# Kernel tuning notes

Hardware: AMD Instinct MI355X
Metric: run time of the kernel (lower is better)

The kernel has to match this reference:

```python
import jax, jax.numpy as jnp
import numpy as np
import math

EMBED_DIM = 256
N_HEAD = 8
N_LEVELS = 4
N_POINTS = 4
HEAD_DIM = EMBED_DIM // N_HEAD
TOTAL_POINTS = N_HEAD * N_LEVELS * N_POINTS
SPATIAL = np.array([[100, 100], [50, 50], [25, 25], [13, 13]], dtype=np.int32)
BS = 2
LEN_Q = int(SPATIAL.prod(1).sum())  # 13294, encoder self-attention
LEN_V = LEN_Q


def setup_inputs() -> dict:
    key = jax.random.key(0)
    ks = jax.random.split(key, 12)
    s = 1.0 / math.sqrt(EMBED_DIM)
    inp = {
        'query': jax.random.normal(ks[0], (BS, LEN_Q, EMBED_DIM), jnp.float32),
        'reference_points': jax.random.uniform(ks[1], (BS, LEN_Q, N_LEVELS, 2), jnp.float32),
        'value': jax.random.normal(ks[2], (BS, LEN_V, EMBED_DIM), jnp.float32),
        'value_spatial_shapes': jnp.asarray(SPATIAL),
        'W_value': jax.random.normal(ks[3], (EMBED_DIM, EMBED_DIM), jnp.float32) * s,
        'b_value': jnp.zeros((EMBED_DIM,), jnp.float32),
        'W_off': jax.random.normal(ks[4], (TOTAL_POINTS * 2, EMBED_DIM), jnp.float32) * 0.01,
        'b_off': jax.random.normal(ks[5], (TOTAL_POINTS * 2,), jnp.float32),
        'W_attn': jax.random.normal(ks[6], (TOTAL_POINTS, EMBED_DIM), jnp.float32) * s,
        'b_attn': jnp.zeros((TOTAL_POINTS,), jnp.float32),
        'W_out': jax.random.normal(ks[7], (EMBED_DIM, EMBED_DIM), jnp.float32) * s,
        'b_out': jnp.zeros((EMBED_DIM,), jnp.float32),
        'zeta': jnp.ones((1, 1, 1, HEAD_DIM), jnp.float32),  # search_type='embed'
    }
    return inp


def _grid_sample_bilinear(img, gx, gy):
    """img: [B,H,W,c]; gx,gy: [B,Q,P] normalized to [-1,1].
    align_corners=False, padding_mode='zeros' (matches F.grid_sample)."""
    B, H, W, c = img.shape
    x = (gx + 1.0) * (0.5 * W) - 0.5
    y = (gy + 1.0) * (0.5 * H) - 0.5
    x0 = jnp.floor(x)
    y0 = jnp.floor(y)
    wx = (x - x0)[..., None]
    wy = (y - y0)[..., None]
    flat = img.reshape(B, H * W, c)

    def gather(xi, yi):
        m = (xi >= 0) & (xi < W) & (yi >= 0) & (yi < H)
        xi_c = jnp.clip(xi, 0, W - 1).astype(jnp.int32)
        yi_c = jnp.clip(yi, 0, H - 1).astype(jnp.int32)
        idx = (yi_c * W + xi_c).reshape(B, -1, 1)
        v = jnp.take_along_axis(flat, idx, axis=1).reshape(B, *xi.shape[1:], c)
        return v * m[..., None]

    v00 = gather(x0, y0)
    v01 = gather(x0 + 1, y0)
    v10 = gather(x0, y0 + 1)
    v11 = gather(x0 + 1, y0 + 1)
    return (v00 * (1 - wx) * (1 - wy) + v01 * wx * (1 - wy)
            + v10 * (1 - wx) * wy + v11 * wx * wy)


def reference(query, reference_points, value, value_spatial_shapes,
              W_value, b_value, W_off, b_off, W_attn, b_attn, W_out, b_out, zeta):
    bs, Len_q, _ = query.shape
    Len_v = value.shape[1]
    shapes = np.asarray(value_spatial_shapes)  # static ints

    # value projection + sparse gate (zeta, not pruned/searched)
    v = value @ W_value.T + b_value
    v = v.reshape(bs, Len_v, N_HEAD, HEAD_DIM) * zeta  # [bs,Lv,h,c]

    # sampling offsets and attention weights from query
    off = (query @ W_off.T + b_off).reshape(bs, Len_q, N_HEAD, N_LEVELS, N_POINTS, 2)
    attn = (query @ W_attn.T + b_attn).reshape(bs, Len_q, N_HEAD, N_LEVELS * N_POINTS)
    attn = jax.nn.softmax(attn, axis=-1).reshape(bs, Len_q, N_HEAD, N_LEVELS, N_POINTS)

    # reference_points last dim == 2 branch
    normalizer = jnp.asarray(shapes[:, ::-1], jnp.float32).reshape(1, 1, 1, N_LEVELS, 1, 2)  # (W,H)
    loc = reference_points.reshape(bs, Len_q, 1, N_LEVELS, 1, 2) + off / normalizer
    grids = 2.0 * loc - 1.0  # [bs,Lq,h,L,P,2]

    B = bs * N_HEAD
    out = jnp.zeros((B, Len_q, HEAD_DIM), jnp.float32)
    start = 0
    for lvl in range(N_LEVELS):
        h, w = int(shapes[lvl, 0]), int(shapes[lvl, 1])
        # [bs, h*w, nh, c] -> [bs*nh, h, w, c]
        v_l = v[:, start:start + h * w].transpose(0, 2, 1, 3).reshape(B, h, w, HEAD_DIM)
        g = grids[:, :, :, lvl].transpose(0, 2, 1, 3, 4).reshape(B, Len_q, N_POINTS, 2)
        samp = _grid_sample_bilinear(v_l, g[..., 0], g[..., 1])  # [B,Lq,P,c]
        a_l = attn[:, :, :, lvl].transpose(0, 2, 1, 3).reshape(B, Len_q, N_POINTS)
        out = out + jnp.einsum('bqpc,bqp->bqc', samp, a_l)
        start += h * w

    out = out.reshape(bs, N_HEAD, Len_q, HEAD_DIM).transpose(0, 2, 1, 3).reshape(bs, Len_q, EMBED_DIM)
    return out @ W_out.T + b_out
```

## Files before the change

### kernel.cpp

```cpp
#include <hip/hip_runtime.h>


#define LQ    13294
#define NTOK  26588
#define NE    6806528

typedef unsigned short ushort_t;
typedef __attribute__((ext_vector_type(8))) short short8;
typedef __attribute__((ext_vector_type(8))) unsigned short ushort8_t;
typedef __attribute__((ext_vector_type(4))) float float4_t;

__device__ __forceinline__ ushort_t f2b(float f) {
    unsigned int x = __float_as_uint(f);
    return (ushort_t)((x + 0x7fffu + ((x >> 16) & 1u)) >> 16);
}

__device__ __forceinline__ void gload16(const void* g, void* l) {
    __builtin_amdgcn_global_load_lds(
        (const __attribute__((address_space(1))) unsigned int*)g,
        (__attribute__((address_space(3))) unsigned int*)l, 16, 0, 0);
}

__device__ __forceinline__ void cvt_seg(const float* __restrict__ s,
                                        ushort_t* __restrict__ d,
                                        int n4, int gid, int stride) {
    const float4_t* s4 = (const float4_t*)s;
    for (int i = gid; i < n4; i += stride) {
        float4_t f = s4[i];
        ushort4 o;
        o.x = f2b(f.x); o.y = f2b(f.y); o.z = f2b(f.z); o.w = f2b(f.w);
        *(ushort4*)(d + (long)i * 4) = o;
    }
}

__global__ __launch_bounds__(256) void cvt_k(
    const float* q, const float* v, const float* Wv, const float* Wo,
    const float* Wa, const float* Wout,
    ushort_t* q_bf, ushort_t* v_bf, ushort_t* Wv_bf, ushort_t* WoWa_bf,
    ushort_t* Wout_bf)
{
    const int gid = blockIdx.x * 256 + threadIdx.x;
    const int stride = gridDim.x * 256;
    cvt_seg(q,    q_bf,            NE / 4,     gid, stride);
    cvt_seg(v,    v_bf,            NE / 4,     gid, stride);
    cvt_seg(Wv,   Wv_bf,           65536 / 4,  gid, stride);
    cvt_seg(Wo,   WoWa_bf,         65536 / 4,  gid, stride);
    cvt_seg(Wa,   WoWa_bf + 65536, 32768 / 4,  gid, stride);
    cvt_seg(Wout, Wout_bf,         65536 / 4,  gid, stride);
}

__device__ __forceinline__ void gemm_tile(
    const ushort_t* __restrict__ A,
    const ushort_t* __restrict__ W,
    int m0, int n0,
    ushort_t* Asb, ushort_t* Bs, float4_t acc[2][4])
{
    const int tid = threadIdx.x;
    const int w  = tid >> 6;
    const int ln = tid & 63;
    const int lr = ln >> 2;
    const int lc = (ln & 3) * 8;

    const ushort_t* gB = W + (long)(n0 + w * 16 + lr) * 256 + lc;
    #pragma unroll
    for (int kt = 0; kt < 8; kt++)
        gload16(gB + kt * 32, Bs + kt * 2048 + w * 512);

    const ushort_t* gA0 = A + (long)(m0 + w * 32 + lr) * 256 + lc;
    const ushort_t* gA1 = gA0 + 16 * 256;
    gload16(gA0, Asb + (w * 2 + 0) * 512);
    gload16(gA1, Asb + (w * 2 + 1) * 512);
    __syncthreads();

    const int krow = (ln >> 4) * 8;
    const int fr   = ln & 15;

    #pragma unroll
    for (int kt = 0; kt < 8; kt++) {
        const int cur = (kt & 1) * 4096;
        if (kt < 7) {
            const int nxt = 4096 - cur;
            gload16(gA0 + (kt + 1) * 32, Asb + nxt + (w * 2 + 0) * 512);
            gload16(gA1 + (kt + 1) * 32, Asb + nxt + (w * 2 + 1) * 512);
        }
        short8 af[2], bfr[4];
        #pragma unroll
        for (int i = 0; i < 2; i++)
            af[i] = *(const short8*)(Asb + cur + (w * 32 + i * 16 + fr) * 32 + krow);
        #pragma unroll
        for (int j = 0; j < 4; j++)
            bfr[j] = *(const short8*)(Bs + kt * 2048 + (j * 16 + fr) * 32 + krow);
        #pragma unroll
        for (int i = 0; i < 2; i++)
            #pragma unroll
            for (int j = 0; j < 4; j++)
                acc[i][j] = __builtin_amdgcn_mfma_f32_16x16x32_bf16(af[i], bfr[j], acc[i][j], 0, 0, 0);
        __syncthreads();
    }
}

__global__ __launch_bounds__(256) void gemm_fused_k(
    const ushort_t* __restrict__ q_bf, const ushort_t* __restrict__ v_bf,
    const ushort_t* __restrict__ Wv,   const ushort_t* __restrict__ WoWa,
    const float* __restrict__ b_value, const float* __restrict__ b_off,
    const float* __restrict__ b_attn,  const float* __restrict__ zeta,
    ushort_t* __restrict__ vproj, float* __restrict__ oa)
{
    __shared__ __align__(16) ushort_t Asb[8192];
    __shared__ __align__(16) ushort_t Bs[16384];

    const int z = blockIdx.z;
    const int bid = blockIdx.x;
    int x, y;
    if (z == 0) {
        if (bid >= 832) return;
        int id = (bid & 7) * 104 + (bid >> 3);
        x = id >> 2; y = id & 3;
    } else {
        int id = (bid & 7) * 156 + (bid >> 3);
        x = id / 6; y = id - x * 6;
    }
    const int m0 = x * 128;
    const int n0 = y * 64;

    float4_t acc[2][4] = {};
    gemm_tile(z ? q_bf : v_bf, z ? WoWa : Wv, m0, n0, Asb, Bs, acc);

    const int tid = threadIdx.x;
    const int w = tid >> 6, ln = tid & 63;
    const int col = ln & 15;
    const int rq  = (ln >> 4) * 4;
    #pragma unroll
    for (int j = 0; j < 4; j++) {
        int n = n0 + j * 16 + col;
        if (z == 0) {
            float bz = b_value[n];
            float zz = zeta[n & 31];
            long hbase = (long)(n >> 5) * NTOK;
            #pragma unroll
            for (int i = 0; i < 2; i++) {
                #pragma unroll
                for (int r = 0; r < 4; r++) {
                    int m = m0 + w * 32 + i * 16 + rq + r;
                    if (m < NTOK)
                        vproj[(hbase + m) * 32 + (n & 31)] = f2b((acc[i][j][r] + bz) * zz);
                }
            }
        } else {
            float bz = (n < 256) ? b_off[n] : b_attn[n - 256];
            #pragma unroll
            for (int i = 0; i < 2; i++) {
                #pragma unroll
                for (int r = 0; r < 4; r++) {
                    int m = m0 + w * 32 + i * 16 + rq + r;
                    if (m < NTOK) oa[(long)m * 384 + n] = acc[i][j][r] + bz;
                }
            }
        }
    }
}

__global__ __launch_bounds__(256) void gemm_out_k(
    const ushort_t* __restrict__ A,
    const ushort_t* __restrict__ W,
    const float* __restrict__ bias,
    float* __restrict__ C)
{
    __shared__ __align__(16) ushort_t Asb[8192];
    __shared__ __align__(16) ushort_t Bs[16384];

    const int bid = blockIdx.x;
    int id = (bid & 7) * 104 + (bid >> 3);
    const int m0 = (id >> 2) * 128;
    const int n0 = (id & 3) * 64;

    float4_t acc[2][4] = {};
    gemm_tile(A, W, m0, n0, Asb, Bs, acc);

    const int tid = threadIdx.x;
    const int w = tid >> 6, ln = tid & 63;
    const int col = ln & 15;
    const int rq  = (ln >> 4) * 4;
    #pragma unroll
    for (int j = 0; j < 4; j++) {
        int n = n0 + j * 16 + col;
        float bz = bias[n];
        #pragma unroll
        for (int i = 0; i < 2; i++) {
            #pragma unroll
            for (int r = 0; r < 4; r++) {
                int m = m0 + w * 32 + i * 16 + rq + r;
                if (m < NTOK) C[(long)m * 256 + n] = acc[i][j][r] + bz;
            }
        }
    }
}

__global__ __launch_bounds__(512) void sample_k(
    const float* __restrict__ refp,
    const ushort_t* __restrict__ v,
    const float* __restrict__ oa,
    ushort_t* __restrict__ outp)
{
    __shared__ __align__(16) int   p_ofs[1152][4];
    __shared__ __align__(16) float p_w[1152][4];
    const int tid = threadIdx.x;
    const int tok = tid >> 6;
    const int ln  = tid & 63;
    const long t  = (long)blockIdx.x * 8 + tok;
    const bool valid = (t < NTOK);
    const int b = (t >= LQ) ? 1 : 0;

    if (valid) {
        #pragma unroll
        for (int half = 0; half < 2; half++) {
            const int h  = (ln >> 4) + half * 4;
            const int pi = ln & 15;
            const int lvl = pi >> 2;
            const int Wi  = (lvl == 0) ? 100 : (lvl == 1) ? 50 : (lvl == 2) ? 25 : 13;
            const int st  = (lvl == 0) ? 0 : (lvl == 1) ? 10000 : (lvl == 2) ? 12500 : 13125;
            const float Wf = (float)Wi;

            float lg = oa[t * 384 + 256 + h * 16 + pi];
            float smax = lg;
            #pragma unroll
            for (int d = 1; d < 16; d <<= 1) smax = fmaxf(smax, __shfl_xor(smax, d, 64));
            float ex = __expf(lg - smax);
            float sm = ex;
            #pragma unroll
            for (int d = 1; d < 16; d <<= 1) sm += __shfl_xor(sm, d, 64);
            const float a = ex / sm;

            float ox = oa[t * 384 + h * 32 + pi * 2];
            float oy = oa[t * 384 + h * 32 + pi * 2 + 1];
            float rx = refp[t * 8 + lvl * 2];
            float ry = refp[t * 8 + lvl * 2 + 1];

            float x = rx * Wf + ox - 0.5f;
            float y = ry * Wf + oy - 0.5f;
            float xf = floorf(x), yf = floorf(y);
            float wx = x - xf, wy = y - yf;
            int x0 = (int)xf, y0 = (int)yf;

            float mx0 = ((unsigned)x0       < (unsigned)Wi) ? (1.f - wx) : 0.f;
            float mx1 = ((unsigned)(x0 + 1) < (unsigned)Wi) ? wx         : 0.f;
            float my0 = ((unsigned)y0       < (unsigned)Wi) ? (1.f - wy) * a : 0.f;
            float my1 = ((unsigned)(y0 + 1) < (unsigned)Wi) ? wy * a         : 0.f;
            int x0c = min(max(x0, 0), Wi - 1);
            int x1c = min(max(x0 + 1, 0), Wi - 1);
            int y0c = min(max(y0, 0), Wi - 1);
            int y1c = min(max(y0 + 1, 0), Wi - 1);

            const int hb = h * NTOK + b * LQ + st;
            int r0 = hb + y0c * Wi, r1 = hb + y1c * Wi;
            const int u  = tok * 128 + half * 64 + ln;
            const int su = u + (u >> 3);
            p_ofs[su][0] = (r0 + x0c) << 6;
            p_ofs[su][1] = (r0 + x1c) << 6;
            p_ofs[su][2] = (r1 + x0c) << 6;
            p_ofs[su][3] = (r1 + x1c) << 6;
            p_w[su][0] = mx0 * my0;
            p_w[su][1] = mx1 * my0;
            p_w[su][2] = mx0 * my1;
            p_w[su][3] = mx1 * my1;
        }
    }
    __syncthreads();

    if (!valid) return;

    const int h = ln >> 3, s = (ln >> 2) & 1, g = ln & 3;
    const char* vb = (const char*)v;
    const unsigned go = g * 16;
    const int base = tok * 128 + h * 16 + s * 8;
    const int skb  = base + (base >> 3);
    float4_t accA = {0.f, 0.f, 0.f, 0.f};
    float4_t accB = {0.f, 0.f, 0.f, 0.f};

    #pragma unroll 2
    for (int p = 0; p < 8; p++) {
        int4     o  = *(const int4*)p_ofs[skb + p];
        float4_t w4 = *(const float4_t*)p_w[skb + p];
        uint4 u00 = *(const uint4*)(vb + (unsigned)(o.x + go));
        uint4 u01 = *(const uint4*)(vb + (unsigned)(o.y + go));
        uint4 u10 = *(const uint4*)(vb + (unsigned)(o.z + go));
        uint4 u11 = *(const uint4*)(vb + (unsigned)(o.w + go));
        #define ACC8(U, WGT) \
            accA[0] += (WGT) * __uint_as_float((U).x << 16); \
            accA[1] += (WGT) * __uint_as_float((U).x & 0xffff0000u); \
            accA[2] += (WGT) * __uint_as_float((U).y << 16); \
            accA[3] += (WGT) * __uint_as_float((U).y & 0xffff0000u); \
            accB[0] += (WGT) * __uint_as_float((U).z << 16); \
            accB[1] += (WGT) * __uint_as_float((U).z & 0xffff0000u); \
            accB[2] += (WGT) * __uint_as_float((U).w << 16); \
            accB[3] += (WGT) * __uint_as_float((U).w & 0xffff0000u);
        ACC8(u00, w4.x)
        ACC8(u01, w4.y)
        ACC8(u10, w4.z)
        ACC8(u11, w4.w)
        #undef ACC8
    }

    #pragma unroll
    for (int c = 0; c < 4; c++) {
        accA[c] += __shfl_down(accA[c], 4, 64);
        accB[c] += __shfl_down(accB[c], 4, 64);
    }

    if ((ln & 4) == 0) {
        ushort8_t o8;
        o8[0] = f2b(accA[0]); o8[1] = f2b(accA[1]);
        o8[2] = f2b(accA[2]); o8[3] = f2b(accA[3]);
        o8[4] = f2b(accB[0]); o8[5] = f2b(accB[1]);
        o8[6] = f2b(accB[2]); o8[7] = f2b(accB[3]);
        *(ushort8_t*)(outp + t * 256 + h * 32 + g * 8) = o8;
    }
}

extern "C" void kernel_launch(void* const* d_in, const int* in_sizes, int n_in,
                              void* d_out, int out_size, void* d_ws, size_t ws_size,
                              hipStream_t stream)
{
    char* ws = (char*)d_ws;
    ushort_t* vproj   = (ushort_t*)ws;
    float*    oa      = (float*)(ws + (long)NE * 2);
    ushort_t* q_bf    = (ushort_t*)(ws + (long)NE * 2 + (long)NTOK * 1536);
    ushort_t* outpre  = q_bf;
    ushort_t* v_bf    = q_bf + NE;
    ushort_t* Wv_bf   = v_bf + NE;
    ushort_t* WoWa_bf = Wv_bf + 65536;
    ushort_t* Wout_bf = WoWa_bf + 98304;

    cvt_k<<<1024, 256, 0, stream>>>(
        (const float*)d_in[0], (const float*)d_in[2], (const float*)d_in[4],
        (const float*)d_in[6], (const float*)d_in[8], (const float*)d_in[10],
        q_bf, v_bf, Wv_bf, WoWa_bf, Wout_bf);

    gemm_fused_k<<<dim3(1248, 1, 2), 256, 0, stream>>>(
        q_bf, v_bf, Wv_bf, WoWa_bf,
        (const float*)d_in[5], (const float*)d_in[7], (const float*)d_in[9],
        (const float*)d_in[12], vproj, oa);

    sample_k<<<3324, 512, 0, stream>>>(
        (const float*)d_in[1], vproj, oa, outpre);

    gemm_out_k<<<832, 256, 0, stream>>>(
        outpre, Wout_bf, (const float*)d_in[11], (float*)d_out);
}
```

Measured before the change: 224.5 us.

## Split sampling kernel per head and simplify GEMM tile staging

The sampling kernel now gives each block one head for eight tokens, so each wave covers one (token, head) pair. Every lane computes its own point's softmax weight, bilinear offsets and four gathers directly, replacing the shared-memory staging of offsets and weights. The per-point partial sums are then reduced across lanes with a shuffle tree, and the grid grows eightfold. Separately, the GEMM tile drops the full B preload and the A double buffering in favour of a plain per-k-step load-sync-compute loop with much smaller LDS buffers, which may raise occupancy but exposes load latency.

```diff
diff --git a/kernel.cpp b/kernel.cpp
--- a/kernel.cpp
+++ b/kernel.cpp
@@ -53,7 +53,7 @@
     const ushort_t* __restrict__ A,
     const ushort_t* __restrict__ W,
     int m0, int n0,
-    ushort_t* Asb, ushort_t* Bs, float4_t acc[2][4])
+    ushort_t* As, ushort_t* Bs, float4_t acc[2][4])
 {
     const int tid = threadIdx.x;
     const int w  = tid >> 6;
@@ -61,35 +61,29 @@
     const int lr = ln >> 2;
     const int lc = (ln & 3) * 8;
 
-    const ushort_t* gB = W + (long)(n0 + w * 16 + lr) * 256 + lc;
-    #pragma unroll
-    for (int kt = 0; kt < 8; kt++)
-        gload16(gB + kt * 32, Bs + kt * 2048 + w * 512);
-
+    ushort_t* lA0 = As + (w * 2 + 0) * 512;
+    ushort_t* lA1 = As + (w * 2 + 1) * 512;
+    ushort_t* lB  = Bs + w * 512;
     const ushort_t* gA0 = A + (long)(m0 + w * 32 + lr) * 256 + lc;
     const ushort_t* gA1 = gA0 + 16 * 256;
-    gload16(gA0, Asb + (w * 2 + 0) * 512);
-    gload16(gA1, Asb + (w * 2 + 1) * 512);
-    __syncthreads();
+    const ushort_t* gB  = W + (long)(n0 + w * 16 + lr) * 256 + lc;
 
     const int krow = (ln >> 4) * 8;
     const int fr   = ln & 15;
 
-    #pragma unroll
-    for (int kt = 0; kt < 8; kt++) {
-        const int cur = (kt & 1) * 4096;
-        if (kt < 7) {
-            const int nxt = 4096 - cur;
-            gload16(gA0 + (kt + 1) * 32, Asb + nxt + (w * 2 + 0) * 512);
-            gload16(gA1 + (kt + 1) * 32, Asb + nxt + (w * 2 + 1) * 512);
-        }
+    for (int k0 = 0; k0 < 256; k0 += 32) {
+        gload16(gA0 + k0, lA0);
+        gload16(gA1 + k0, lA1);
+        gload16(gB  + k0, lB);
+        __syncthreads();
+
         short8 af[2], bfr[4];
         #pragma unroll
         for (int i = 0; i < 2; i++)
-            af[i] = *(const short8*)(Asb + cur + (w * 32 + i * 16 + fr) * 32 + krow);
+            af[i] = *(const short8*)(As + (w * 32 + i * 16 + fr) * 32 + krow);
         #pragma unroll
         for (int j = 0; j < 4; j++)
-            bfr[j] = *(const short8*)(Bs + kt * 2048 + (j * 16 + fr) * 32 + krow);
+            bfr[j] = *(const short8*)(Bs + (j * 16 + fr) * 32 + krow);
         #pragma unroll
         for (int i = 0; i < 2; i++)
             #pragma unroll
@@ -106,8 +100,8 @@
     const float* __restrict__ b_attn,  const float* __restrict__ zeta,
     ushort_t* __restrict__ vproj, float* __restrict__ oa)
 {
-    __shared__ __align__(16) ushort_t Asb[8192];
-    __shared__ __align__(16) ushort_t Bs[16384];
+    __shared__ __align__(16) ushort_t As[128 * 32];
+    __shared__ __align__(16) ushort_t Bs[64 * 32];
 
     const int z = blockIdx.z;
     const int bid = blockIdx.x;
@@ -124,7 +118,7 @@
     const int n0 = y * 64;
 
     float4_t acc[2][4] = {};
-    gemm_tile(z ? q_bf : v_bf, z ? WoWa : Wv, m0, n0, Asb, Bs, acc);
+    gemm_tile(z ? q_bf : v_bf, z ? WoWa : Wv, m0, n0, As, Bs, acc);
 
     const int tid = threadIdx.x;
     const int w = tid >> 6, ln = tid & 63;
@@ -166,8 +160,8 @@
     const float* __restrict__ bias,
     float* __restrict__ C)
 {
-    __shared__ __align__(16) ushort_t Asb[8192];
-    __shared__ __align__(16) ushort_t Bs[16384];
+    __shared__ __align__(16) ushort_t As[128 * 32];
+    __shared__ __align__(16) ushort_t Bs[64 * 32];
 
     const int bid = blockIdx.x;
     int id = (bid & 7) * 104 + (bid >> 3);
@@ -175,7 +169,7 @@
     const int n0 = (id & 3) * 64;
 
     float4_t acc[2][4] = {};
-    gemm_tile(A, W, m0, n0, Asb, Bs, acc);
+    gemm_tile(A, W, m0, n0, As, Bs, acc);
 
     const int tid = threadIdx.x;
     const int w = tid >> 6, ln = tid & 63;
@@ -202,112 +196,88 @@
     const float* __restrict__ oa,
     ushort_t* __restrict__ outp)
 {
-    __shared__ __align__(16) int   p_ofs[1152][4];
-    __shared__ __align__(16) float p_w[1152][4];
+    const int bid = blockIdx.x;
+    const int h   = bid & 7;
     const int tid = threadIdx.x;
-    const int tok = tid >> 6;
-    const int ln  = tid & 63;
-    const long t  = (long)blockIdx.x * 8 + tok;
-    const bool valid = (t < NTOK);
-    const int b = (t >= LQ) ? 1 : 0;
-
-    if (valid) {
-        #pragma unroll
-        for (int half = 0; half < 2; half++) {
-            const int h  = (ln >> 4) + half * 4;
-            const int pi = ln & 15;
-            const int lvl = pi >> 2;
-            const int Wi  = (lvl == 0) ? 100 : (lvl == 1) ? 50 : (lvl == 2) ? 25 : 13;
-            const int st  = (lvl == 0) ? 0 : (lvl == 1) ? 10000 : (lvl == 2) ? 12500 : 13125;
-            const float Wf = (float)Wi;
-
-            float lg = oa[t * 384 + 256 + h * 16 + pi];
-            float smax = lg;
-            #pragma unroll
-            for (int d = 1; d < 16; d <<= 1) smax = fmaxf(smax, __shfl_xor(smax, d, 64));
-            float ex = __expf(lg - smax);
-            float sm = ex;
-            #pragma unroll
-            for (int d = 1; d < 16; d <<= 1) sm += __shfl_xor(sm, d, 64);
-            const float a = ex / sm;
-
-            float ox = oa[t * 384 + h * 32 + pi * 2];
-            float oy = oa[t * 384 + h * 32 + pi * 2 + 1];
-            float rx = refp[t * 8 + lvl * 2];
-            float ry = refp[t * 8 + lvl * 2 + 1];
-
-            float x = rx * Wf + ox - 0.5f;
-            float y = ry * Wf + oy - 0.5f;
-            float xf = floorf(x), yf = floorf(y);
-            float wx = x - xf, wy = y - yf;
-            int x0 = (int)xf, y0 = (int)yf;
-
-            float mx0 = ((unsigned)x0       < (unsigned)Wi) ? (1.f - wx) : 0.f;
-            float mx1 = ((unsigned)(x0 + 1) < (unsigned)Wi) ? wx         : 0.f;
-            float my0 = ((unsigned)y0       < (unsigned)Wi) ? (1.f - wy) * a : 0.f;
-            float my1 = ((unsigned)(y0 + 1) < (unsigned)Wi) ? wy * a         : 0.f;
-            int x0c = min(max(x0, 0), Wi - 1);
-            int x1c = min(max(x0 + 1, 0), Wi - 1);
-            int y0c = min(max(y0, 0), Wi - 1);
-            int y1c = min(max(y0 + 1, 0), Wi - 1);
-
-            const int hb = h * NTOK + b * LQ + st;
-            int r0 = hb + y0c * Wi, r1 = hb + y1c * Wi;
-            const int u  = tok * 128 + half * 64 + ln;
-            const int su = u + (u >> 3);
-            p_ofs[su][0] = (r0 + x0c) << 6;
-            p_ofs[su][1] = (r0 + x1c) << 6;
-            p_ofs[su][2] = (r1 + x0c) << 6;
-            p_ofs[su][3] = (r1 + x1c) << 6;
-            p_w[su][0] = mx0 * my0;
-            p_w[su][1] = mx1 * my0;
-            p_w[su][2] = mx0 * my1;
-            p_w[su][3] = mx1 * my1;
-        }
-    }
-    __syncthreads();
-
-    if (!valid) return;
-
-    const int h = ln >> 3, s = (ln >> 2) & 1, g = ln & 3;
+    const long t  = (long)(bid >> 3) * 8 + (tid >> 6);
+    if (t >= NTOK) return;
+    const int b  = (t >= LQ) ? 1 : 0;
+    const int ln = tid & 63;
+    const int p  = ln >> 2, g = ln & 3;
+    const int lvl = p >> 2;
+    const int Wi  = (lvl == 0) ? 100 : (lvl == 1) ? 50 : (lvl == 2) ? 25 : 13;
+    const int st  = (lvl == 0) ? 0 : (lvl == 1) ? 10000 : (lvl == 2) ? 12500 : 13125;
+    const float Wf = (float)Wi;
+
+    float lg = oa[t * 384 + 256 + h * 16 + p];
+    float smax = lg;
+    #pragma unroll
+    for (int d = 4; d < 64; d <<= 1) smax = fmaxf(smax, __shfl_xor(smax, d, 64));
+    float ex = __expf(lg - smax);
+    float sm = ex;
+    #pragma unroll
+    for (int d = 4; d < 64; d <<= 1) sm += __shfl_xor(sm, d, 64);
+    const float a = ex / sm;
+
+    float ox = oa[t * 384 + h * 32 + p * 2];
+    float oy = oa[t * 384 + h * 32 + p * 2 + 1];
+    float rx = refp[t * 8 + lvl * 2];
+    float ry = refp[t * 8 + lvl * 2 + 1];
+
+    float x = rx * Wf + ox - 0.5f;
+    float y = ry * Wf + oy - 0.5f;
+    float xf = floorf(x), yf = floorf(y);
+    float wx = x - xf, wy = y - yf;
+    int x0 = (int)xf, y0 = (int)yf;
+
+    float mx0 = ((unsigned)x0       < (unsigned)Wi) ? (1.f - wx) : 0.f;
+    float mx1 = ((unsigned)(x0 + 1) < (unsigned)Wi) ? wx         : 0.f;
+    float my0 = ((unsigned)y0       < (unsigned)Wi) ? (1.f - wy) * a : 0.f;
+    float my1 = ((unsigned)(y0 + 1) < (unsigned)Wi) ? wy * a         : 0.f;
+    int x0c = min(max(x0, 0), Wi - 1);
+    int x1c = min(max(x0 + 1, 0), Wi - 1);
+    int y0c = min(max(y0, 0), Wi - 1);
+    int y1c = min(max(y0 + 1, 0), Wi - 1);
+
+    const int hb = h * NTOK + b * LQ + st;
+    const int go = g * 16;
+    const int r0 = hb + y0c * Wi, r1 = hb + y1c * Wi;
     const char* vb = (const char*)v;
-    const unsigned go = g * 16;
-    const int base = tok * 128 + h * 16 + s * 8;
-    const int skb  = base + (base >> 3);
+    uint4 u00 = *(const uint4*)(vb + (((r0 + x0c) << 6) + go));
+    uint4 u01 = *(const uint4*)(vb + (((r0 + x1c) << 6) + go));
+    uint4 u10 = *(const uint4*)(vb + (((r1 + x0c) << 6) + go));
+    uint4 u11 = *(const uint4*)(vb + (((r1 + x1c) << 6) + go));
+
+    const float w00 = mx0 * my0, w01 = mx1 * my0;
+    const float w10 = mx0 * my1, w11 = mx1 * my1;
+
     float4_t accA = {0.f, 0.f, 0.f, 0.f};
     float4_t accB = {0.f, 0.f, 0.f, 0.f};
-
-    #pragma unroll 2
-    for (int p = 0; p < 8; p++) {
-        int4     o  = *(const int4*)p_ofs[skb + p];
-        float4_t w4 = *(const float4_t*)p_w[skb + p];
-        uint4 u00 = *(const uint4*)(vb + (unsigned)(o.x + go));
-        uint4 u01 = *(const uint4*)(vb + (unsigned)(o.y + go));
-        uint4 u10 = *(const uint4*)(vb + (unsigned)(o.z + go));
-        uint4 u11 = *(const uint4*)(vb + (unsigned)(o.w + go));
-        #define ACC8(U, WGT) \
-            accA[0] += (WGT) * __uint_as_float((U).x << 16); \
-            accA[1] += (WGT) * __uint_as_float((U).x & 0xffff0000u); \
-            accA[2] += (WGT) * __uint_as_float((U).y << 16); \
-            accA[3] += (WGT) * __uint_as_float((U).y & 0xffff0000u); \
-            accB[0] += (WGT) * __uint_as_float((U).z << 16); \
-            accB[1] += (WGT) * __uint_as_float((U).z & 0xffff0000u); \
-            accB[2] += (WGT) * __uint_as_float((U).w << 16); \
-            accB[3] += (WGT) * __uint_as_float((U).w & 0xffff0000u);
-        ACC8(u00, w4.x)
-        ACC8(u01, w4.y)
-        ACC8(u10, w4.z)
-        ACC8(u11, w4.w)
-        #undef ACC8
-    }
-
-    #pragma unroll
-    for (int c = 0; c < 4; c++) {
-        accA[c] += __shfl_down(accA[c], 4, 64);
-        accB[c] += __shfl_down(accB[c], 4, 64);
-    }
-
-    if ((ln & 4) == 0) {
+    #define ACC8(U, WGT) \
+        accA[0] += (WGT) * __uint_as_float((U).x << 16); \
+        accA[1] += (WGT) * __uint_as_float((U).x & 0xffff0000u); \
+        accA[2] += (WGT) * __uint_as_float((U).y << 16); \
+        accA[3] += (WGT) * __uint_as_float((U).y & 0xffff0000u); \
+        accB[0] += (WGT) * __uint_as_float((U).z << 16); \
+        accB[1] += (WGT) * __uint_as_float((U).z & 0xffff0000u); \
+        accB[2] += (WGT) * __uint_as_float((U).w << 16); \
+        accB[3] += (WGT) * __uint_as_float((U).w & 0xffff0000u);
+    ACC8(u00, w00)
+    ACC8(u01, w01)
+    ACC8(u10, w10)
+    ACC8(u11, w11)
+    #undef ACC8
+
+    #pragma unroll
+    for (int d = 32; d >= 4; d >>= 1) {
+        #pragma unroll
+        for (int c = 0; c < 4; c++) {
+            accA[c] += __shfl_down(accA[c], d, 64);
+            accB[c] += __shfl_down(accB[c], d, 64);
+        }
+    }
+
+    if (p == 0) {
         ushort8_t o8;
         o8[0] = f2b(accA[0]); o8[1] = f2b(accA[1]);
         o8[2] = f2b(accA[2]); o8[3] = f2b(accA[3]);
@@ -341,7 +311,7 @@
         (const float*)d_in[5], (const float*)d_in[7], (const float*)d_in[9],
         (const float*)d_in[12], vproj, oa);
 
-    sample_k<<<3324, 512, 0, stream>>>(
+    sample_k<<<8 * 3324, 512, 0, stream>>>(
         (const float*)d_in[1], vproj, oa, outpre);
 
     gemm_out_k<<<832, 256, 0, stream>>>(
```

Result: slower. 243.5 us (+8.5%).
